# Performance work log

Measured on AMD Instinct MI355X. Metric: run time of the kernel, lower is better.

The kernel has to match this reference:

```python
import jax, jax.numpy as jnp
import numpy as np

DECAY = 0.8
EPS = 1e-05


def setup_inputs() -> dict:
    key = jax.random.key(0)
    k1, k2, k3 = jax.random.split(key, 3)
    b, n, d = 16, 4096, 64
    h, c = 1, 2048
    x = jax.random.normal(k1, (b, n, d), dtype=jnp.float32)
    embeddings = jax.random.normal(k2, (h, c, d), dtype=jnp.float32)
    cluster_size = jnp.ones((h, c), dtype=jnp.float32)
    embed_avg = jax.random.normal(k3, (h, c, d), dtype=jnp.float32)
    return {"x": x, "embeddings": embeddings, "cluster_size": cluster_size, "embed_avg": embed_avg}


def reference(x, embeddings, cluster_size, embed_avg):
    # x: (b, n, d); add codebook dim h=1 and flatten -> (h, N, d)
    d = x.shape[-1]
    flat = x.reshape(1, -1, d)                              # (h, N, d)
    h, C = embeddings.shape[0], embeddings.shape[1]

    # dist = -cdist(flat, embeddings)  (negative euclidean distance)
    x2 = jnp.sum(flat * flat, axis=-1, keepdims=True)       # (h, N, 1)
    e2 = jnp.sum(embeddings * embeddings, axis=-1)          # (h, C)
    xe = jnp.einsum('hnd,hcd->hnc', flat, embeddings)       # (h, N, C)
    dist = -jnp.sqrt(jnp.clip(x2 + e2[:, None, :] - 2.0 * xe, 0.0))

    # gumbel_sample with stochastic=False, straight_through=False -> hard argmax
    embed_ind = jnp.argmax(dist, axis=-1)                   # (h, N)

    # quantize: gather selected codes
    quantize = jnp.take_along_axis(embeddings, embed_ind[..., None], axis=1)  # (h, N, d)

    # EMA codebook update (scatter-based): counts and per-code feature sums
    counts = jax.vmap(lambda i: jnp.bincount(i, length=C))(embed_ind).astype(x.dtype)  # (h, C)
    embed_sum = jax.vmap(lambda f, i: jax.ops.segment_sum(f, i, num_segments=C))(flat, embed_ind)  # (h, C, d)

    new_cluster_size = cluster_size * DECAY + counts * (1.0 - DECAY)
    new_embed_avg = embed_avg * DECAY + embed_sum * (1.0 - DECAY)

    # laplace smoothing of cluster sizes, then renormalize embed_avg
    tot = jnp.sum(new_cluster_size, axis=-1, keepdims=True)
    smoothed = (new_cluster_size + EPS) / (tot + C * EPS) * tot
    new_embeddings = new_embed_avg / smoothed[..., None]

    quantize = quantize.reshape(x.shape)                    # drop h dim back to (b, n, d)
    embed_ind = embed_ind.reshape(x.shape[:-1])             # (b, n)
    return quantize, embed_ind, new_embeddings, new_cluster_size, new_embed_avg
```

## Files before the change

### kernel.cpp

```cpp
#include <hip/hip_runtime.h>

#define N_TOK 65536
#define D 64
#define C_CODES 2048
#define DECAYF 0.8f
#define OMDF 0.2f
#define EPSF 1e-5f
#define SEG 16
#define GAP_THR 0.0625f
#define TCODES 32
#define NTILES (C_CODES / TCODES)

#define OUT_QUANT 0
#define OUT_IND   (N_TOK * D)
#define OUT_EMB   (OUT_IND + N_TOK)
#define OUT_CS    (OUT_EMB + C_CODES * D)
#define OUT_EAVG  (OUT_CS + C_CODES)

typedef short s16x8 __attribute__((ext_vector_type(8)));
typedef float f32x4 __attribute__((ext_vector_type(4)));

__device__ __forceinline__ unsigned short f2bf(float f) {
    unsigned int u = __float_as_uint(f);
    return (unsigned short)((u + 0x7fffu + ((u >> 16) & 1u)) >> 16);
}
__device__ __forceinline__ float bf2f(unsigned short h) {
    return __uint_as_float(((unsigned int)h) << 16);
}
__device__ __forceinline__ unsigned long long shflx64w(unsigned long long v, int mask, int w) {
    unsigned int lo = (unsigned int)v, hi = (unsigned int)(v >> 32);
    lo = __shfl_xor(lo, mask, w);
    hi = __shfl_xor(hi, mask, w);
    return ((unsigned long long)hi << 32) | lo;
}
__device__ __forceinline__ void gload_lds16(const void* g, void* l) {
    __builtin_amdgcn_global_load_lds(
        (const __attribute__((address_space(1))) void*)g,
        (__attribute__((address_space(3))) void*)l, 16, 0, 0);
}

__global__ void eprep_kernel(const float* __restrict__ emb, short* __restrict__ ebk,
                             float* __restrict__ e2, unsigned int* __restrict__ e2p,
                             float* __restrict__ counts, float* __restrict__ embed_sum,
                             int* __restrict__ pend_n) {
    int g = blockIdx.x * blockDim.x + threadIdx.x;
    int code = g >> 3, slot = g & 7;
    int kc = slot ^ (code & 7);
    const float4* ep = (const float4*)(emb + (size_t)code * D + kc * 8);
    float4 a = ep[0], b = ep[1];
    float v[8] = {a.x, a.y, a.z, a.w, b.x, b.y, b.z, b.w};
    s16x8 h, l;
#pragma unroll
    for (int j = 0; j < 8; ++j) {
        unsigned short hb = f2bf(v[j]);
        h[j] = (short)hb;
        l[j] = (short)f2bf(v[j] - bf2f(hb));
    }
    *(s16x8*)(ebk + (size_t)code * 128 + slot * 8) = h;
    *(s16x8*)(ebk + (size_t)code * 128 + 64 + slot * 8) = l;

    float4 z = {0.f, 0.f, 0.f, 0.f};
    ((float4*)embed_sum)[g * 2] = z;
    ((float4*)embed_sum)[g * 2 + 1] = z;
    if (g < C_CODES / 4) ((float4*)counts)[g] = z;
    if (g == 0) pend_n[0] = 0;

    if (g < C_CODES) {
        const float4* er = (const float4*)(emb + (size_t)g * D);
        float s0 = 0.f, s1 = 0.f, s2 = 0.f, s3 = 0.f;
#pragma unroll
        for (int i = 0; i < D / 4; ++i) {
            float4 e = er[i];
            s0 = fmaf(e.x, e.x, s0);
            s1 = fmaf(e.y, e.y, s1);
            s2 = fmaf(e.z, e.z, s2);
            s3 = fmaf(e.w, e.w, s3);
        }
        float vv = (s0 + s1) + (s2 + s3);
        e2[g] = vv;
        unsigned short hb = f2bf(vv);
        unsigned short lb = f2bf(vv - bf2f(hb));
        e2p[g] = (unsigned int)hb | ((unsigned int)lb << 16);
    }
}

__global__ __launch_bounds__(256) void screen_kernel(
        const float* __restrict__ x, const float* __restrict__ emb,
        const short* __restrict__ ebk, const float* __restrict__ e2,
        const unsigned int* __restrict__ e2p,
        int* __restrict__ idx, float* __restrict__ out, float* __restrict__ counts,
        int* __restrict__ pend_n, unsigned int* __restrict__ pend) {
    __shared__ unsigned int e2pl[C_CODES];
    __shared__ __align__(16) char bstage[2][TCODES * 256];
    __shared__ unsigned int fin[4][32][5];

    const int tid = threadIdx.x;
    ((uint4*)e2pl)[tid] = ((const uint4*)e2p)[tid];
    ((uint4*)e2pl)[tid + 256] = ((const uint4*)e2p)[tid + 256];

    const int lane = tid & 63;
    const int wave = tid >> 6;
    const int col = lane & 15;
    const int krow = lane >> 4;

    s16x8 ah[2][2], al[2][2];
#pragma unroll
    for (int s = 0; s < 2; ++s) {
        int tok = blockIdx.x * 128 + wave * 32 + s * 16 + col;
        const float4* xp = (const float4*)(x + (size_t)tok * D + krow * 8);
        float4 f0 = xp[0], f1 = xp[1], f2 = xp[8], f3 = xp[9];
        float xv[16] = {f0.x, f0.y, f0.z, f0.w, f1.x, f1.y, f1.z, f1.w,
                        f2.x, f2.y, f2.z, f2.w, f3.x, f3.y, f3.z, f3.w};
#pragma unroll
        for (int j = 0; j < 8; ++j) {
            float v0 = -2.0f * xv[j];
            unsigned short h0 = f2bf(v0);
            ah[s][0][j] = (short)h0;
            al[s][0][j] = (short)f2bf(v0 - bf2f(h0));
            float v1 = -2.0f * xv[8 + j];
            unsigned short h1 = f2bf(v1);
            ah[s][1][j] = (short)h1;
            al[s][1][j] = (short)f2bf(v1 - bf2f(h1));
        }
    }

    s16x8 aone = {0, 0, 0, 0, 0, 0, 0, 0};
    {
        short o = (krow == 0) ? (short)0x3F80 : (short)0;
        aone[0] = o;
        aone[1] = o;
    }
    const f32x4 zero = {0.f, 0.f, 0.f, 0.f};

    float b1[2][4], b2[2][4], b3[2][4];
    unsigned int c1[2][4], c2[2][4];
#pragma unroll
    for (int s = 0; s < 2; ++s)
#pragma unroll
        for (int r = 0; r < 4; ++r) {
            b1[s][r] = __builtin_inff();
            b2[s][r] = __builtin_inff();
            b3[s][r] = __builtin_inff();
            c1[s][r] = 0u;
            c2[s][r] = 0u;
        }

    auto stage = [&](int b, int t) {
        const char* src = (const char*)ebk + (size_t)t * (TCODES * 256)
                          + wave * 2048 + lane * 16;
        char* dst = &bstage[b][wave * 2048];
        gload_lds16(src, dst);
        gload_lds16(src + 1024, dst + 1024);
    };

    auto subtile = [&](const char* lb, int t, int j) {
        const char* base = lb + (j << 12) + (col << 8);
        int off = (krow ^ (col & 7)) << 4;
        s16x8 bh0 = *(const s16x8*)(base + off);
        s16x8 bh1 = *(const s16x8*)(base + (off ^ 64));
        s16x8 bl0 = *(const s16x8*)(base + 128 + off);
        s16x8 bl1 = *(const s16x8*)(base + 128 + (off ^ 64));
        int sloc = t * 2 + j;
        unsigned int cg = (unsigned int)(sloc * 16 + col);
        unsigned int v = e2pl[sloc * 16 + col];
        v = (krow == 0) ? v : 0u;
        s16x8 be2 = {(short)(v & 0xffffu), (short)(v >> 16), 0, 0, 0, 0, 0, 0};
        f32x4 f = __builtin_amdgcn_mfma_f32_16x16x32_bf16(aone, be2, zero, 0, 0, 0);
#pragma unroll
        for (int s = 0; s < 2; ++s) {
            f32x4 acc = __builtin_amdgcn_mfma_f32_16x16x32_bf16(ah[s][1], bh1, f, 0, 0, 0);
            acc = __builtin_amdgcn_mfma_f32_16x16x32_bf16(ah[s][0], bh0, acc, 0, 0, 0);
            acc = __builtin_amdgcn_mfma_f32_16x16x32_bf16(al[s][1], bh1, acc, 0, 0, 0);
            acc = __builtin_amdgcn_mfma_f32_16x16x32_bf16(al[s][0], bh0, acc, 0, 0, 0);
            acc = __builtin_amdgcn_mfma_f32_16x16x32_bf16(ah[s][1], bl1, acc, 0, 0, 0);
            acc = __builtin_amdgcn_mfma_f32_16x16x32_bf16(ah[s][0], bl0, acc, 0, 0, 0);
#pragma unroll
            for (int r = 0; r < 4; ++r) {
                float sc = acc[r];
                bool l1 = sc < b1[s][r];
                bool l2 = sc < b2[s][r];
                b3[s][r] = __builtin_amdgcn_fmed3f(b2[s][r], b3[s][r], sc);
                b2[s][r] = __builtin_amdgcn_fmed3f(b1[s][r], b2[s][r], sc);
                unsigned int tc = l1 ? c1[s][r] : cg;
                c2[s][r] = l2 ? tc : c2[s][r];
                b1[s][r] = fminf(b1[s][r], sc);
                c1[s][r] = l1 ? cg : c1[s][r];
            }
        }
    };

    stage(0, 0);
    __syncthreads();

    for (int t = 0; t < NTILES; ++t) {
        if (t + 1 < NTILES) stage((t + 1) & 1, t + 1);
        const char* lb = bstage[t & 1];
        subtile(lb, t, 0);
        subtile(lb, t, 1);
        __syncthreads();
    }

#pragma unroll
    for (int s = 0; s < 2; ++s)
#pragma unroll
        for (int r = 0; r < 4; ++r) {
            float B1 = b1[s][r], B2 = b2[s][r], B3 = b3[s][r];
            unsigned int C1 = c1[s][r], C2 = c2[s][r];
#pragma unroll
            for (int mk = 1; mk < 16; mk <<= 1) {
                float o1 = __shfl_xor(B1, mk, 16);
                float o2 = __shfl_xor(B2, mk, 16);
                float o3 = __shfl_xor(B3, mk, 16);
                unsigned int oc1 = (unsigned int)__shfl_xor((int)C1, mk, 16);
                unsigned int oc2 = (unsigned int)__shfl_xor((int)C2, mk, 16);
                bool ta = B1 <= o1;
                float x1v = ta ? o1 : B1;
                unsigned int xc = ta ? oc1 : C1;
                float nm1 = ta ? B1 : o1;
                unsigned int nc1 = ta ? C1 : oc1;
                bool tb = B2 <= o2;
                float y1v = tb ? B2 : o2;
                unsigned int yc = tb ? C2 : oc2;
                bool tc = x1v <= y1v;
                float nm2 = tc ? x1v : y1v;
                unsigned int nc2 = tc ? xc : yc;
                float nm3 = fminf(fmaxf(x1v, y1v), fminf(B3, o3));
                B1 = nm1; C1 = nc1; B2 = nm2; C2 = nc2; B3 = nm3;
            }
            if (col == 0) {
                int tl = s * 16 + krow * 4 + r;
                fin[wave][tl][0] = __float_as_uint(B1);
                fin[wave][tl][1] = C1;
                fin[wave][tl][2] = __float_as_uint(B2);
                fin[wave][tl][3] = C2;
                fin[wave][tl][4] = __float_as_uint(B3);
            }
        }
    __syncthreads();

    if (lane < 32) {
        const unsigned int* f = fin[wave][lane];
        float m1 = __uint_as_float(f[0]);
        int cm1 = (int)f[1];
        float m2 = __uint_as_float(f[2]);
        int cm2 = (int)f[3];
        float m3 = __uint_as_float(f[4]);
        int tok = blockIdx.x * 128 + wave * 32 + lane;
        bool uniq = (m2 - m1 > GAP_THR);
        bool pairf = !uniq && (m3 - m1 > GAP_THR);
        int c = cm1;

        if (pairf) {
            int ca = cm1, cb = cm2;
            float xs[4] = {0.f, 0.f, 0.f, 0.f};
            float da[4] = {0.f, 0.f, 0.f, 0.f};
            float db[4] = {0.f, 0.f, 0.f, 0.f};
            for (int q = 0; q < 4; ++q) {
                const float4* xq = (const float4*)(x + (size_t)tok * D + q * 16);
                const float4* ea = (const float4*)(emb + (size_t)ca * D + q * 16);
                const float4* eb = (const float4*)(emb + (size_t)cb * D + q * 16);
#pragma unroll
                for (int j = 0; j < 4; ++j) {
                    float4 xv = xq[j], av = ea[j], bv = eb[j];
                    xs[0] = fmaf(xv.x, xv.x, xs[0]);
                    xs[1] = fmaf(xv.y, xv.y, xs[1]);
                    xs[2] = fmaf(xv.z, xv.z, xs[2]);
                    xs[3] = fmaf(xv.w, xv.w, xs[3]);
                    da[0] = fmaf(xv.x, av.x, da[0]);
                    da[1] = fmaf(xv.y, av.y, da[1]);
                    da[2] = fmaf(xv.z, av.z, da[2]);
                    da[3] = fmaf(xv.w, av.w, da[3]);
                    db[0] = fmaf(xv.x, bv.x, db[0]);
                    db[1] = fmaf(xv.y, bv.y, db[1]);
                    db[2] = fmaf(xv.z, bv.z, db[2]);
                    db[3] = fmaf(xv.w, bv.w, db[3]);
                }
            }
            float x2 = (xs[0] + xs[1]) + (xs[2] + xs[3]);
            float dota = (da[0] + da[1]) + (da[2] + da[3]);
            float dA = fmaxf(x2 + e2[ca] - 2.0f * dota, 0.0f);
            float dotb = (db[0] + db[1]) + (db[2] + db[3]);
            float dB = fmaxf(x2 + e2[cb] - 2.0f * dotb, 0.0f);
            unsigned long long ka =
                ((unsigned long long)__float_as_uint(dA) << 32) | (unsigned int)ca;
            unsigned long long kb =
                ((unsigned long long)__float_as_uint(dB) << 32) | (unsigned int)cb;
            c = (int)((ka < kb ? ka : kb) & 0xffffffffull);
        }

        if (uniq || pairf) {
            idx[tok] = c;
            out[OUT_IND + tok] = (float)c;
            atomicAdd(&counts[c], 1.0f);
            const float4* er = (const float4*)(emb + (size_t)c * D);
            float4* qo = (float4*)(out + OUT_QUANT) + (size_t)tok * 16;
#pragma unroll
            for (int q = 0; q < 16; ++q) qo[q] = er[q];
        } else {
            int p = atomicAdd(pend_n, 1);
            pend[p] = (unsigned int)tok;
        }
    }
}

__global__ __launch_bounds__(256) void cleanup_kernel(
        const float* __restrict__ x, const float* __restrict__ emb,
        const float* __restrict__ e2, const int* __restrict__ pend_n,
        const unsigned int* __restrict__ pend,
        int* __restrict__ idx, float* __restrict__ out, float* __restrict__ counts) {
    int gw = (int)((blockIdx.x * blockDim.x + threadIdx.x) >> 6);
    int nw = (int)((gridDim.x * blockDim.x) >> 6);
    int lane = threadIdx.x & 63;
    int M = pend_n[0];
    for (int i = gw; i < M; i += nw) {
        int tn = (int)pend[i];
        float xs[4] = {0.f, 0.f, 0.f, 0.f};
        for (int q = 0; q < 4; ++q) {
            const float4* xq = (const float4*)(x + (size_t)tn * D + q * 16);
#pragma unroll
            for (int j = 0; j < 4; ++j) {
                float4 xv = xq[j];
                xs[0] = fmaf(xv.x, xv.x, xs[0]);
                xs[1] = fmaf(xv.y, xv.y, xs[1]);
                xs[2] = fmaf(xv.z, xv.z, xs[2]);
                xs[3] = fmaf(xv.w, xv.w, xs[3]);
            }
        }
        float tx2 = (xs[0] + xs[1]) + (xs[2] + xs[3]);
        unsigned long long kbest = ~0ull;
        for (int cc = lane; cc < C_CODES; cc += 64) {
            float d0 = 0.f, d1 = 0.f, d2 = 0.f, d3 = 0.f;
            for (int q = 0; q < 4; ++q) {
                const float4* xq = (const float4*)(x + (size_t)tn * D + q * 16);
                const float4* er = (const float4*)(emb + (size_t)cc * D + q * 16);
#pragma unroll
                for (int j = 0; j < 4; ++j) {
                    float4 xv = xq[j], ev = er[j];
                    d0 = fmaf(xv.x, ev.x, d0);
                    d1 = fmaf(xv.y, ev.y, d1);
                    d2 = fmaf(xv.z, ev.z, d2);
                    d3 = fmaf(xv.w, ev.w, d3);
                }
            }
            float dot = (d0 + d1) + (d2 + d3);
            float dist2 = fmaxf(tx2 + e2[cc] - 2.0f * dot, 0.0f);
            unsigned long long key =
                ((unsigned long long)__float_as_uint(dist2) << 32) | (unsigned int)cc;
            kbest = key < kbest ? key : kbest;
        }
#pragma unroll
        for (int mk = 1; mk < 64; mk <<= 1) {
            unsigned long long o = shflx64w(kbest, mk, 64);
            kbest = o < kbest ? o : kbest;
        }
        int c = (int)(kbest & 0xffffffffull);
        out[OUT_QUANT + (size_t)tn * D + lane] = emb[(size_t)c * D + lane];
        if (lane == 0) {
            idx[tn] = c;
            out[OUT_IND + tn] = (float)c;
            atomicAdd(&counts[c], 1.0f);
        }
    }
}

__global__ void prefix_ema_kernel(const float* __restrict__ counts,
                                  const float* __restrict__ cluster_size,
                                  float* __restrict__ out,
                                  float* __restrict__ smoothed,
                                  int* __restrict__ cursor) {
    __shared__ float scan[256];
    __shared__ float red[256];
    int t = threadIdx.x;
    int base = t * 8;
    float cnt[8], ncs[8];
    float csum = 0.f, nsum = 0.f;
#pragma unroll
    for (int j = 0; j < 8; ++j) {
        cnt[j] = counts[base + j];
        csum += cnt[j];
        ncs[j] = cluster_size[base + j] * DECAYF + cnt[j] * OMDF;
        nsum += ncs[j];
        out[OUT_CS + base + j] = ncs[j];
    }
    scan[t] = csum;
    red[t] = nsum;
    __syncthreads();
    for (int s = 1; s < 256; s <<= 1) {
        float v = scan[t];
        float w = (t >= s) ? scan[t - s] : 0.f;
        __syncthreads();
        scan[t] = v + w;
        __syncthreads();
    }
    for (int s = 128; s > 0; s >>= 1) {
        if (t < s) red[t] += red[t + s];
        __syncthreads();
    }
    float tot = red[0];
    float run = (t == 0) ? 0.f : scan[t - 1];
#pragma unroll
    for (int j = 0; j < 8; ++j) {
        cursor[base + j] = (int)run;
        run += cnt[j];
        smoothed[base + j] = (ncs[j] + EPSF) / (tot + (float)C_CODES * EPSF) * tot;
    }
}

__global__ void scatter_pos_kernel(const int* __restrict__ idx,
                                   int* __restrict__ cursor,
                                   unsigned int* __restrict__ sorted) {
    int n = blockIdx.x * blockDim.x + threadIdx.x;
    int c = idx[n];
    int pos = atomicAdd(&cursor[c], 1);
    sorted[pos] = ((unsigned int)c << 16) | (unsigned int)n;
}

__global__ __launch_bounds__(256) void seg_sum_kernel(
        const float* __restrict__ x, const unsigned int* __restrict__ sorted,
        float* __restrict__ embed_sum) {
    int lane = threadIdx.x & 63;
    int q = blockIdx.x * 4 + (threadIdx.x >> 6);
    int p0 = q * SEG;

    unsigned int mine = (lane < SEG) ? sorted[p0 + lane] : 0u;
    unsigned int pk[SEG];
#pragma unroll
    for (int j = 0; j < SEG; ++j) pk[j] = __shfl(mine, j, 64);

    float xv[SEG];
#pragma unroll
    for (int j = 0; j < SEG; ++j)
        xv[j] = x[(size_t)(pk[j] & 0xffffu) * D + lane];

    unsigned int run_c = 0xffffffffu;
    float sum = 0.f;
#pragma unroll
    for (int j = 0; j < SEG; ++j) {
        unsigned int c = pk[j] >> 16;
        if (c != run_c) {
            if (run_c != 0xffffffffu)
                atomicAdd(&embed_sum[(size_t)run_c * D + lane], sum);
            run_c = c;
            sum = 0.f;
        }
        sum += xv[j];
    }
    atomicAdd(&embed_sum[(size_t)run_c * D + lane], sum);
}

__global__ void ema_embed_kernel(const float* __restrict__ embed_avg,
                                 const float* __restrict__ embed_sum,
                                 const float* __restrict__ smoothed,
                                 float* __restrict__ out) {
    int g = blockIdx.x * blockDim.x + threadIdx.x;
    int c = g >> 4;
    float4 ea = ((const float4*)embed_avg)[g];
    float4 es = ((const float4*)embed_sum)[g];
    float4 na;
    na.x = ea.x * DECAYF + es.x * OMDF;
    na.y = ea.y * DECAYF + es.y * OMDF;
    na.z = ea.z * DECAYF + es.z * OMDF;
    na.w = ea.w * DECAYF + es.w * OMDF;
    ((float4*)(out + OUT_EAVG))[g] = na;
    float sm = smoothed[c];
    float4 ne;
    ne.x = na.x / sm;
    ne.y = na.y / sm;
    ne.z = na.z / sm;
    ne.w = na.w / sm;
    ((float4*)(out + OUT_EMB))[g] = ne;
}

extern "C" void kernel_launch(void* const* d_in, const int* in_sizes, int n_in,
                              void* d_out, int out_size, void* d_ws, size_t ws_size,
                              hipStream_t stream) {
    const float* x            = (const float*)d_in[0];
    const float* emb          = (const float*)d_in[1];
    const float* cluster_size = (const float*)d_in[2];
    const float* embed_avg    = (const float*)d_in[3];
    float* out = (float*)d_out;

    float* e2        = (float*)d_ws;
    unsigned int* e2p = (unsigned int*)(e2 + C_CODES);
    float* counts    = (float*)(e2p + C_CODES);
    float* smoothed  = counts + C_CODES;
    int*   cursor    = (int*)(smoothed + C_CODES);
    int*   idx       = cursor + C_CODES;
    unsigned int* sorted = (unsigned int*)(idx + N_TOK);
    int*   pend_n    = (int*)(sorted + N_TOK);
    unsigned int* pend = (unsigned int*)(pend_n + 4);
    float* embed_sum = (float*)(pend + N_TOK);
    short* ebk       = (short*)(embed_sum + C_CODES * D);

    eprep_kernel<<<(C_CODES * 8) / 256, 256, 0, stream>>>(emb, ebk, e2, e2p, counts,
                                                          embed_sum, pend_n);
    screen_kernel<<<N_TOK / 128, 256, 0, stream>>>(x, emb, ebk, e2, e2p, idx, out,
                                                   counts, pend_n, pend);
    cleanup_kernel<<<128, 256, 0, stream>>>(x, emb, e2, pend_n, pend, idx, out, counts);
    prefix_ema_kernel<<<1, 256, 0, stream>>>(counts, cluster_size, out, smoothed, cursor);
    scatter_pos_kernel<<<N_TOK / 256, 256, 0, stream>>>(idx, cursor, sorted);
    seg_sum_kernel<<<(N_TOK / SEG) / 4, 256, 0, stream>>>(x, sorted, embed_sum);
    ema_embed_kernel<<<(C_CODES * 16) / 256, 256, 0, stream>>>(embed_avg, embed_sum,
                                                              smoothed, out);
}
```

Measured before the change: 274.9 us.

## Halve tokens per screen block and coalesce quantize gather through shared memory

The screen kernel now gives each wave 16 tokens instead of 32, which doubles the grid to 1024 blocks so more of them can be resident at once. The cost is that every block restages the whole codebook, so codebook traffic and LDS staging double relative to compute. The quantize output copy moves out of the per-thread path into a cooperative gather: chosen code indices are stored in shared memory, then all 64 lanes write contiguous float4 rows. Bounds clamps are added on the pending-list index and count as a safety measure.

Result: faster. 260.3 us (-5.3%).

```diff
diff --git a/kernel.cpp b/kernel.cpp
--- a/kernel.cpp
+++ b/kernel.cpp
@@ -10,6 +10,7 @@
 #define GAP_THR 0.0625f
 #define TCODES 32
 #define NTILES (C_CODES / TCODES)
+#define BLKTOK 64
 
 #define OUT_QUANT 0
 #define OUT_IND   (N_TOK * D)
@@ -92,7 +93,7 @@
         int* __restrict__ pend_n, unsigned int* __restrict__ pend) {
     __shared__ unsigned int e2pl[C_CODES];
     __shared__ __align__(16) char bstage[2][TCODES * 256];
-    __shared__ unsigned int fin[4][32][5];
+    __shared__ unsigned int fin[4][16][5];
 
     const int tid = threadIdx.x;
     ((uint4*)e2pl)[tid] = ((const uint4*)e2p)[tid];
@@ -103,10 +104,9 @@
     const int col = lane & 15;
     const int krow = lane >> 4;
 
-    s16x8 ah[2][2], al[2][2];
-#pragma unroll
-    for (int s = 0; s < 2; ++s) {
-        int tok = blockIdx.x * 128 + wave * 32 + s * 16 + col;
+    s16x8 ah0, ah1, al0, al1;
+    {
+        int tok = blockIdx.x * BLKTOK + wave * 16 + col;
         const float4* xp = (const float4*)(x + (size_t)tok * D + krow * 8);
         float4 f0 = xp[0], f1 = xp[1], f2 = xp[8], f3 = xp[9];
         float xv[16] = {f0.x, f0.y, f0.z, f0.w, f1.x, f1.y, f1.z, f1.w,
@@ -115,12 +115,12 @@
         for (int j = 0; j < 8; ++j) {
             float v0 = -2.0f * xv[j];
             unsigned short h0 = f2bf(v0);
-            ah[s][0][j] = (short)h0;
-            al[s][0][j] = (short)f2bf(v0 - bf2f(h0));
+            ah0[j] = (short)h0;
+            al0[j] = (short)f2bf(v0 - bf2f(h0));
             float v1 = -2.0f * xv[8 + j];
             unsigned short h1 = f2bf(v1);
-            ah[s][1][j] = (short)h1;
-            al[s][1][j] = (short)f2bf(v1 - bf2f(h1));
+            ah1[j] = (short)h1;
+            al1[j] = (short)f2bf(v1 - bf2f(h1));
         }
     }
 
@@ -132,18 +132,16 @@
     }
     const f32x4 zero = {0.f, 0.f, 0.f, 0.f};
 
-    float b1[2][4], b2[2][4], b3[2][4];
-    unsigned int c1[2][4], c2[2][4];
-#pragma unroll
-    for (int s = 0; s < 2; ++s)
-#pragma unroll
-        for (int r = 0; r < 4; ++r) {
-            b1[s][r] = __builtin_inff();
-            b2[s][r] = __builtin_inff();
-            b3[s][r] = __builtin_inff();
-            c1[s][r] = 0u;
-            c2[s][r] = 0u;
-        }
+    float b1[4], b2[4], b3[4];
+    unsigned int c1[4], c2[4];
+#pragma unroll
+    for (int r = 0; r < 4; ++r) {
+        b1[r] = __builtin_inff();
+        b2[r] = __builtin_inff();
+        b3[r] = __builtin_inff();
+        c1[r] = 0u;
+        c2[r] = 0u;
+    }
 
     auto stage = [&](int b, int t) {
         const char* src = (const char*)ebk + (size_t)t * (TCODES * 256)
@@ -166,26 +164,23 @@
         v = (krow == 0) ? v : 0u;
         s16x8 be2 = {(short)(v & 0xffffu), (short)(v >> 16), 0, 0, 0, 0, 0, 0};
         f32x4 f = __builtin_amdgcn_mfma_f32_16x16x32_bf16(aone, be2, zero, 0, 0, 0);
-#pragma unroll
-        for (int s = 0; s < 2; ++s) {
-            f32x4 acc = __builtin_amdgcn_mfma_f32_16x16x32_bf16(ah[s][1], bh1, f, 0, 0, 0);
-            acc = __builtin_amdgcn_mfma_f32_16x16x32_bf16(ah[s][0], bh0, acc, 0, 0, 0);
-            acc = __builtin_amdgcn_mfma_f32_16x16x32_bf16(al[s][1], bh1, acc, 0, 0, 0);
-            acc = __builtin_amdgcn_mfma_f32_16x16x32_bf16(al[s][0], bh0, acc, 0, 0, 0);
-            acc = __builtin_amdgcn_mfma_f32_16x16x32_bf16(ah[s][1], bl1, acc, 0, 0, 0);
-            acc = __builtin_amdgcn_mfma_f32_16x16x32_bf16(ah[s][0], bl0, acc, 0, 0, 0);
-#pragma unroll
-            for (int r = 0; r < 4; ++r) {
-                float sc = acc[r];
-                bool l1 = sc < b1[s][r];
-                bool l2 = sc < b2[s][r];
-                b3[s][r] = __builtin_amdgcn_fmed3f(b2[s][r], b3[s][r], sc);
-                b2[s][r] = __builtin_amdgcn_fmed3f(b1[s][r], b2[s][r], sc);
-                unsigned int tc = l1 ? c1[s][r] : cg;
-                c2[s][r] = l2 ? tc : c2[s][r];
-                b1[s][r] = fminf(b1[s][r], sc);
-                c1[s][r] = l1 ? cg : c1[s][r];
-            }
+        f32x4 acc = __builtin_amdgcn_mfma_f32_16x16x32_bf16(ah1, bh1, f, 0, 0, 0);
+        acc = __builtin_amdgcn_mfma_f32_16x16x32_bf16(ah0, bh0, acc, 0, 0, 0);
+        acc = __builtin_amdgcn_mfma_f32_16x16x32_bf16(al1, bh1, acc, 0, 0, 0);
+        acc = __builtin_amdgcn_mfma_f32_16x16x32_bf16(al0, bh0, acc, 0, 0, 0);
+        acc = __builtin_amdgcn_mfma_f32_16x16x32_bf16(ah1, bl1, acc, 0, 0, 0);
+        acc = __builtin_amdgcn_mfma_f32_16x16x32_bf16(ah0, bl0, acc, 0, 0, 0);
+#pragma unroll
+        for (int r = 0; r < 4; ++r) {
+            float sc = acc[r];
+            bool l1 = sc < b1[r];
+            bool l2 = sc < b2[r];
+            b3[r] = __builtin_amdgcn_fmed3f(b2[r], b3[r], sc);
+            b2[r] = __builtin_amdgcn_fmed3f(b1[r], b2[r], sc);
+            unsigned int tc = l1 ? c1[r] : cg;
+            c2[r] = l2 ? tc : c2[r];
+            b1[r] = fminf(b1[r], sc);
+            c1[r] = l1 ? cg : c1[r];
         }
     };
 
@@ -201,51 +196,49 @@
     }
 
 #pragma unroll
-    for (int s = 0; s < 2; ++s)
-#pragma unroll
-        for (int r = 0; r < 4; ++r) {
-            float B1 = b1[s][r], B2 = b2[s][r], B3 = b3[s][r];
-            unsigned int C1 = c1[s][r], C2 = c2[s][r];
-#pragma unroll
-            for (int mk = 1; mk < 16; mk <<= 1) {
-                float o1 = __shfl_xor(B1, mk, 16);
-                float o2 = __shfl_xor(B2, mk, 16);
-                float o3 = __shfl_xor(B3, mk, 16);
-                unsigned int oc1 = (unsigned int)__shfl_xor((int)C1, mk, 16);
-                unsigned int oc2 = (unsigned int)__shfl_xor((int)C2, mk, 16);
-                bool ta = B1 <= o1;
-                float x1v = ta ? o1 : B1;
-                unsigned int xc = ta ? oc1 : C1;
-                float nm1 = ta ? B1 : o1;
-                unsigned int nc1 = ta ? C1 : oc1;
-                bool tb = B2 <= o2;
-                float y1v = tb ? B2 : o2;
-                unsigned int yc = tb ? C2 : oc2;
-                bool tc = x1v <= y1v;
-                float nm2 = tc ? x1v : y1v;
-                unsigned int nc2 = tc ? xc : yc;
-                float nm3 = fminf(fmaxf(x1v, y1v), fminf(B3, o3));
-                B1 = nm1; C1 = nc1; B2 = nm2; C2 = nc2; B3 = nm3;
-            }
-            if (col == 0) {
-                int tl = s * 16 + krow * 4 + r;
-                fin[wave][tl][0] = __float_as_uint(B1);
-                fin[wave][tl][1] = C1;
-                fin[wave][tl][2] = __float_as_uint(B2);
-                fin[wave][tl][3] = C2;
-                fin[wave][tl][4] = __float_as_uint(B3);
-            }
-        }
+    for (int r = 0; r < 4; ++r) {
+        float B1 = b1[r], B2 = b2[r], B3 = b3[r];
+        unsigned int C1 = c1[r], C2 = c2[r];
+#pragma unroll
+        for (int mk = 1; mk < 16; mk <<= 1) {
+            float o1 = __shfl_xor(B1, mk, 16);
+            float o2 = __shfl_xor(B2, mk, 16);
+            float o3 = __shfl_xor(B3, mk, 16);
+            unsigned int oc1 = (unsigned int)__shfl_xor((int)C1, mk, 16);
+            unsigned int oc2 = (unsigned int)__shfl_xor((int)C2, mk, 16);
+            bool ta = B1 <= o1;
+            float x1v = ta ? o1 : B1;
+            unsigned int xc = ta ? oc1 : C1;
+            float nm1 = ta ? B1 : o1;
+            unsigned int nc1 = ta ? C1 : oc1;
+            bool tb = B2 <= o2;
+            float y1v = tb ? B2 : o2;
+            unsigned int yc = tb ? C2 : oc2;
+            bool tc = x1v <= y1v;
+            float nm2 = tc ? x1v : y1v;
+            unsigned int nc2 = tc ? xc : yc;
+            float nm3 = fminf(fmaxf(x1v, y1v), fminf(B3, o3));
+            B1 = nm1; C1 = nc1; B2 = nm2; C2 = nc2; B3 = nm3;
+        }
+        if (col == 0) {
+            int tl = krow * 4 + r;
+            fin[wave][tl][0] = __float_as_uint(B1);
+            fin[wave][tl][1] = C1;
+            fin[wave][tl][2] = __float_as_uint(B2);
+            fin[wave][tl][3] = C2;
+            fin[wave][tl][4] = __float_as_uint(B3);
+        }
+    }
     __syncthreads();
 
-    if (lane < 32) {
+    if (lane < 16) {
         const unsigned int* f = fin[wave][lane];
         float m1 = __uint_as_float(f[0]);
         int cm1 = (int)f[1];
         float m2 = __uint_as_float(f[2]);
         int cm2 = (int)f[3];
         float m3 = __uint_as_float(f[4]);
-        int tok = blockIdx.x * 128 + wave * 32 + lane;
+        int tok = blockIdx.x * BLKTOK + wave * 16 + lane;
         bool uniq = (m2 - m1 > GAP_THR);
         bool pairf = !uniq && (m3 - m1 > GAP_THR);
         int c = cm1;
@@ -292,13 +285,24 @@
             idx[tok] = c;
             out[OUT_IND + tok] = (float)c;
             atomicAdd(&counts[c], 1.0f);
-            const float4* er = (const float4*)(emb + (size_t)c * D);
-            float4* qo = (float4*)(out + OUT_QUANT) + (size_t)tok * 16;
-#pragma unroll
-            for (int q = 0; q < 16; ++q) qo[q] = er[q];
         } else {
             int p = atomicAdd(pend_n, 1);
-            pend[p] = (unsigned int)tok;
+            if (p >= 0 && p < N_TOK) pend[p] = (unsigned int)tok;
+        }
+        fin[wave][lane][1] = (unsigned int)c;
+    }
+    __syncthreads();
+
+    {
+        int t0 = blockIdx.x * BLKTOK + wave * 16;
+        float4* qo = (float4*)(out + OUT_QUANT + (size_t)t0 * D);
+#pragma unroll
+        for (int j = 0; j < 4; ++j) {
+            int o = j * 64 + lane;
+            int tl = o >> 4;
+            int d4 = o & 15;
+            int c = (int)fin[wave][tl][1];
+            qo[o] = ((const float4*)(emb + (size_t)c * D))[d4];
         }
     }
 }
@@ -312,8 +316,9 @@
     int nw = (int)((gridDim.x * blockDim.x) >> 6);
     int lane = threadIdx.x & 63;
     int M = pend_n[0];
+    M = (M < 0) ? 0 : ((M > N_TOK) ? N_TOK : M);
     for (int i = gw; i < M; i += nw) {
-        int tn = (int)pend[i];
+        int tn = (int)(pend[i] & 0xffffu);
         float xs[4] = {0.f, 0.f, 0.f, 0.f};
         for (int q = 0; q < 4; ++q) {
             const float4* xq = (const float4*)(x + (size_t)tn * D + q * 16);
@@ -494,8 +499,8 @@
 
     eprep_kernel<<<(C_CODES * 8) / 256, 256, 0, stream>>>(emb, ebk, e2, e2p, counts,
                                                           embed_sum, pend_n);
-    screen_kernel<<<N_TOK / 128, 256, 0, stream>>>(x, emb, ebk, e2, e2p, idx, out,
-                                                   counts, pend_n, pend);
+    screen_kernel<<<N_TOK / BLKTOK, 256, 0, stream>>>(x, emb, ebk, e2, e2p, idx, out,
+                                                      counts, pend_n, pend);
     cleanup_kernel<<<128, 256, 0, stream>>>(x, emb, e2, pend_n, pend, idx, out, counts);
     prefix_ema_kernel<<<1, 256, 0, stream>>>(counts, cluster_size, out, smoothed, cursor);
     scatter_pos_kernel<<<N_TOK / 256, 256, 0, stream>>>(idx, cursor, sorted);
```
